# Kernel optimization log

Measured on AMD Instinct MI355X. Metric: run time of the kernel, lower is better.

Reference implementation:

```python
import jax, jax.numpy as jnp
import numpy as np

WINDOW_SIZE = 11
CHANNEL = 3
DATA_RANGE = 1.0
C1 = (0.01 * DATA_RANGE) ** 2
C2 = (0.03 * DATA_RANGE) ** 2


def _gaussian_window(window_size, channel, sigma=1.5):
    coords = np.arange(window_size, dtype=np.float32) - window_size // 2
    g = np.exp(-coords ** 2 / (2 * sigma ** 2))
    g = g / g.sum()
    g2d = g[:, None] * g[None, :]  # [K, K]
    # depthwise conv weight in OIHW with groups=channel -> [C, 1, K, K]
    w = np.broadcast_to(g2d[None, None], (channel, 1, window_size, window_size))
    return jnp.asarray(np.ascontiguousarray(w))


def _dwconv(x, w):
    # depthwise conv, stride 1, SAME padding (== pad window//2 for odd kernel)
    return jax.lax.conv_general_dilated(
        x, w, window_strides=(1, 1), padding='SAME',
        feature_group_count=x.shape[1],
        dimension_numbers=('NCHW', 'OIHW', 'NCHW'))


def setup_inputs() -> dict:
    key = jax.random.key(0)
    k1, k2 = jax.random.split(key)
    img1 = jax.random.normal(k1, (32, 3, 512, 512), dtype=jnp.float32)
    img2 = jax.random.normal(k2, (32, 3, 512, 512), dtype=jnp.float32)
    window = _gaussian_window(WINDOW_SIZE, CHANNEL)
    return {"img1": img1, "img2": img2, "window": window}


def reference(img1, img2, window):
    mu1 = _dwconv(img1, window)
    mu2 = _dwconv(img2, window)
    mu1_sq = mu1 * mu1
    mu2_sq = mu2 * mu2
    mu1_mu2 = mu1 * mu2
    sigma1_sq = jnp.maximum(_dwconv(img1 * img1, window) - mu1_sq, 0.0)
    sigma2_sq = jnp.maximum(_dwconv(img2 * img2, window) - mu2_sq, 0.0)
    sigma12 = _dwconv(img1 * img2, window) - mu1_mu2
    s1 = jnp.sqrt(sigma1_sq)
    s2 = jnp.sqrt(sigma2_sq)
    luminance = (2.0 * mu1_mu2 + C1) / (mu1_sq + mu2_sq + C1)
    contrast = (2.0 * s1 * s2 + C2) / (sigma1_sq + sigma2_sq + C2)
    structure = (sigma12 + C2 / 2) / (s1 * s2 + C2 / 2)
    ssim_map = luminance * contrast * structure
    return jnp.mean(ssim_map)
```

## Files before the change

### kernel.cpp

```cpp
#include <hip/hip_runtime.h>


#define IMG_H 512
#define IMG_W 512
#define N_IMGS 96
#define WAVE_W 64
#define STRIPE 128
#define HALO 5
#define KW 11
#define IN_COLS (WAVE_W + 2*HALO)
#define N_ROWT (IMG_H / STRIPE)
#define N_COLT (IMG_W / WAVE_W)
#define N_TILES (N_IMGS * N_ROWT * N_COLT)
#define WPB 4
#define N_BLOCKS (N_TILES / WPB)
#define T_MAX 143
#define NBINS 256
#define TOTAL_PIX (32.0f * 3.0f * 512.0f * 512.0f)

__global__ __launch_bounds__(64 * WPB)
void ssim_main(
    const float* __restrict__ img1, const float* __restrict__ img2,
    const float* __restrict__ window, float* __restrict__ bins)
{
    __shared__ float2 rowbuf_all[WPB][2][IN_COLS + 2];

    const int lane = threadIdx.x & 63;
    const int wv   = threadIdx.x >> 6;
    float2 (* __restrict__ rowbuf)[IN_COLS + 2] = rowbuf_all[wv];

    float g[KW];
    {
        const float inv = rsqrtf(window[5*KW + 5]);
        #pragma unroll
        for (int k = 0; k < KW; ++k)
            g[k] = __int_as_float(
                __builtin_amdgcn_readfirstlane(
                    __float_as_int(window[5*KW + k] * inv)));
    }

    const int b   = blockIdx.x * WPB + wv;
    const int img = b >> 5;
    const int rem = b & 31;
    const int ty  = rem >> 3;
    const int tx  = rem & 7;
    const int r0  = ty * STRIPE;
    const int x0  = tx * WAVE_W;

    const float* __restrict__ p1 = img1 + (size_t)img * (IMG_H * IMG_W);
    const float* __restrict__ p2 = img2 + (size_t)img * (IMG_H * IMG_W);

    const int  gx1  = x0 - HALO + lane;
    const bool c1ok = (unsigned)gx1 < IMG_W;
    const bool tail = lane < (IN_COLS - WAVE_W);
    const int  gx2  = gx1 + WAVE_W;
    const bool c2ok = tail && ((unsigned)gx2 < IMG_W);

    float r_h1[KW], r_h2[KW], r_h11[KW], r_h22[KW], r_h12[KW];
    #pragma unroll
    for (int i = 0; i < KW; ++i) {
        r_h1[i] = 0.f; r_h2[i] = 0.f; r_h11[i] = 0.f; r_h22[i] = 0.f; r_h12[i] = 0.f;
    }

    const float C1 = 1e-4f;
    const float C2 = 9e-4f;
    float sum = 0.f;

    float sa = 0.f, sb = 0.f, sa2 = 0.f, sb2 = 0.f;
    {
        const int gy = r0 - HALO;
        if ((unsigned)gy < IMG_H) {
            const int base = gy * IMG_W;
            if (c1ok) { sa  = p1[base + gx1]; sb  = p2[base + gx1]; }
            if (c2ok) { sa2 = p1[base + gx2]; sb2 = p2[base + gx2]; }
        }
    }

    #pragma unroll 1
    for (int tb = 0; tb < T_MAX; tb += KW) {
        #pragma unroll
        for (int u = 0; u < KW; ++u) {
            const int t = tb + u;

            rowbuf[u & 1][lane] = make_float2(sa, sb);
            if (tail) rowbuf[u & 1][lane + WAVE_W] = make_float2(sa2, sb2);

            asm volatile("" ::: "memory");

            {
                const int gy = r0 - HALO + t + 1;
                sa = 0.f; sb = 0.f; sa2 = 0.f; sb2 = 0.f;
                if ((unsigned)gy < IMG_H) {
                    const int base = gy * IMG_W;
                    if (c1ok) { sa  = p1[base + gx1]; sb  = p2[base + gx1]; }
                    if (c2ok) { sa2 = p1[base + gx2]; sb2 = p2[base + gx2]; }
                }
            }

            float h1 = 0.f, h2 = 0.f, h11 = 0.f, h22 = 0.f, h12 = 0.f;
            #pragma unroll
            for (int k = 0; k < KW; ++k) {
                const float2 v = rowbuf[u & 1][lane + k];
                const float t1 = g[k] * v.x;
                const float t2 = g[k] * v.y;
                h1  += t1;
                h2  += t2;
                h11 += t1 * v.x;
                h22 += t2 * v.y;
                h12 += t1 * v.y;
            }
            r_h1[u] = h1; r_h2[u] = h2; r_h11[u] = h11; r_h22[u] = h22; r_h12[u] = h12;

            if (t >= 2*HALO && t < 2*HALO + STRIPE) {
                float mu1 = 0.f, mu2 = 0.f, e11 = 0.f, e22 = 0.f, e12 = 0.f;
                #pragma unroll
                for (int m = 0; m < KW; ++m) {
                    const int slot = (u + 1 + m) % KW;
                    mu1 += g[m] * r_h1[slot];
                    mu2 += g[m] * r_h2[slot];
                    e11 += g[m] * r_h11[slot];
                    e22 += g[m] * r_h22[slot];
                    e12 += g[m] * r_h12[slot];
                }
                const float mu1s = mu1 * mu1, mu2s = mu2 * mu2, mu12 = mu1 * mu2;
                const float s1  = fmaxf(e11 - mu1s, 0.f);
                const float s2  = fmaxf(e22 - mu2s, 0.f);
                const float s12 = e12 - mu12;
                const float num = (2.f * mu12 + C1) * (2.f * s12 + C2);
                const float den = (mu1s + mu2s + C1) * (s1 + s2 + C2);
                sum += num * __builtin_amdgcn_rcpf(den);
            }
        }
    }

    #pragma unroll
    for (int off = 32; off > 0; off >>= 1)
        sum += __shfl_down(sum, off, 64);
    if (lane == 0)
        atomicAdd(&bins[b & (NBINS - 1)], sum);
}

__global__ __launch_bounds__(64) void ssim_final(
    const float* __restrict__ bins, float* __restrict__ out)
{
    const int tid = threadIdx.x;
    float s = 0.f;
    #pragma unroll
    for (int i = 0; i < NBINS / 64; ++i) s += bins[tid + i * 64];
    #pragma unroll
    for (int off = 32; off > 0; off >>= 1)
        s += __shfl_down(s, off, 64);
    if (tid == 0) out[0] = s * (1.0f / TOTAL_PIX);
}

extern "C" void kernel_launch(void* const* d_in, const int* in_sizes, int n_in,
                              void* d_out, int out_size, void* d_ws, size_t ws_size,
                              hipStream_t stream) {
    const float* img1   = (const float*)d_in[0];
    const float* img2   = (const float*)d_in[1];
    const float* window = (const float*)d_in[2];
    float* bins = (float*)d_ws;
    float* out  = (float*)d_out;

    hipMemsetAsync(bins, 0, NBINS * sizeof(float), stream);
    ssim_main<<<N_BLOCKS, 64 * WPB, 0, stream>>>(img1, img2, window, bins);
    ssim_final<<<1, 64, 0, stream>>>(bins, out);
}
```

Baseline: 318.7 us.

## Stream rows directly into LDS with async global_load_lds and 4-slot ring

Replaces register-staged row loads with direct global-to-LDS async loads (global_load_lds) into a 4-deep ring buffer, prefetching three rows ahead and waiting on vmcnt. Column indices are clamped and out-of-range halo columns are zeroed explicitly at image edges, while rows outside the image issue dummy loads to keep the vmcnt accounting constant. The row layout also changes from interleaved float2 to separate planes per image. The aim is deeper memory-latency hiding and less VGPR/LDS store traffic, at the cost of reliance on hand-coded waitcnt counts and races between zero-fill stores and in-flight async writes.

```diff
diff --git a/kernel.cpp b/kernel.cpp
--- a/kernel.cpp
+++ b/kernel.cpp
@@ -1,17 +1,16 @@
 #include <hip/hip_runtime.h>
+#include <stdint.h>
 
 
 #define IMG_H 512
 #define IMG_W 512
-#define N_IMGS 96
 #define WAVE_W 64
 #define STRIPE 128
 #define HALO 5
 #define KW 11
-#define IN_COLS (WAVE_W + 2*HALO)
 #define N_ROWT (IMG_H / STRIPE)
 #define N_COLT (IMG_W / WAVE_W)
-#define N_TILES (N_IMGS * N_ROWT * N_COLT)
+#define N_TILES (96 * N_ROWT * N_COLT)
 #define WPB 4
 #define N_BLOCKS (N_TILES / WPB)
 #define T_MAX 143
@@ -23,11 +22,13 @@
     const float* __restrict__ img1, const float* __restrict__ img2,
     const float* __restrict__ window, float* __restrict__ bins)
 {
-    __shared__ float2 rowbuf_all[WPB][2][IN_COLS + 2];
+    __shared__ float buf_all[WPB][4][2][128];
+    __shared__ float dump_all[WPB][64];
 
     const int lane = threadIdx.x & 63;
     const int wv   = threadIdx.x >> 6;
-    float2 (* __restrict__ rowbuf)[IN_COLS + 2] = rowbuf_all[wv];
+    float (* __restrict__ buf)[2][128] = buf_all[wv];
+    float* __restrict__ dump = dump_all[wv];
 
     float g[KW];
     {
@@ -50,11 +51,34 @@
     const float* __restrict__ p1 = img1 + (size_t)img * (IMG_H * IMG_W);
     const float* __restrict__ p2 = img2 + (size_t)img * (IMG_H * IMG_W);
 
-    const int  gx1  = x0 - HALO + lane;
-    const bool c1ok = (unsigned)gx1 < IMG_W;
-    const bool tail = lane < (IN_COLS - WAVE_W);
-    const int  gx2  = gx1 + WAVE_W;
-    const bool c2ok = tail && ((unsigned)gx2 < IMG_W);
+    const int cm = min(max(x0 - HALO + lane, 0), IMG_W - 1);
+    const int ct = min(max(x0 + WAVE_W - HALO + lane, 0), IMG_W - 1);
+
+    const float* pm1 = p1 + (long)(r0 - HALO) * IMG_W + cm;
+    const float* pm2 = p2 + (long)(r0 - HALO) * IMG_W + cm;
+    const float* pt1 = p1 + (long)(r0 - HALO) * IMG_W + ct;
+    const float* pt2 = p2 + (long)(r0 - HALO) * IMG_W + ct;
+    const float* pdm = p1 + lane;
+
+    auto issue = [&](int tl) {
+        const int slot = tl & 3;
+        float* s0 = &buf[slot][0][0];
+        float* s1 = &buf[slot][1][0];
+        if ((unsigned)(r0 - HALO + tl) < IMG_H) {
+            __builtin_amdgcn_global_load_lds(pm1, s0,      4, 0, 0);
+            __builtin_amdgcn_global_load_lds(pt1, s0 + 64, 4, 0, 0);
+            __builtin_amdgcn_global_load_lds(pm2, s1,      4, 0, 0);
+            __builtin_amdgcn_global_load_lds(pt2, s1 + 64, 4, 0, 0);
+        } else {
+            __builtin_amdgcn_global_load_lds(pdm, dump, 4, 0, 0);
+            __builtin_amdgcn_global_load_lds(pdm, dump, 4, 0, 0);
+            __builtin_amdgcn_global_load_lds(pdm, dump, 4, 0, 0);
+            __builtin_amdgcn_global_load_lds(pdm, dump, 4, 0, 0);
+            s0[lane] = 0.f; s0[64 + lane] = 0.f;
+            s1[lane] = 0.f; s1[64 + lane] = 0.f;
+        }
+        pm1 += IMG_W; pm2 += IMG_W; pt1 += IMG_W; pt2 += IMG_W;
+    };
 
     float r_h1[KW], r_h2[KW], r_h11[KW], r_h22[KW], r_h12[KW];
     #pragma unroll
@@ -66,15 +90,7 @@
     const float C2 = 9e-4f;
     float sum = 0.f;
 
-    float sa = 0.f, sb = 0.f, sa2 = 0.f, sb2 = 0.f;
-    {
-        const int gy = r0 - HALO;
-        if ((unsigned)gy < IMG_H) {
-            const int base = gy * IMG_W;
-            if (c1ok) { sa  = p1[base + gx1]; sb  = p2[base + gx1]; }
-            if (c2ok) { sa2 = p1[base + gx2]; sb2 = p2[base + gx2]; }
-        }
-    }
+    issue(0); issue(1); issue(2);
 
     #pragma unroll 1
     for (int tb = 0; tb < T_MAX; tb += KW) {
@@ -82,33 +98,40 @@
         for (int u = 0; u < KW; ++u) {
             const int t = tb + u;
 
-            rowbuf[u & 1][lane] = make_float2(sa, sb);
-            if (tail) rowbuf[u & 1][lane + WAVE_W] = make_float2(sa2, sb2);
+            issue(t + 3);
 
-            asm volatile("" ::: "memory");
+            asm volatile("s_waitcnt vmcnt(12)" ::: "memory");
 
-            {
-                const int gy = r0 - HALO + t + 1;
-                sa = 0.f; sb = 0.f; sa2 = 0.f; sb2 = 0.f;
-                if ((unsigned)gy < IMG_H) {
-                    const int base = gy * IMG_W;
-                    if (c1ok) { sa  = p1[base + gx1]; sb  = p2[base + gx1]; }
-                    if (c2ok) { sa2 = p1[base + gx2]; sb2 = p2[base + gx2]; }
+            if (tx == 0) {
+                if (lane < HALO) {
+                    buf[t & 3][0][lane] = 0.f;
+                    buf[t & 3][1][lane] = 0.f;
+                }
+            }
+            if (tx == 7) {
+                if (lane >= HALO && lane < 2*HALO) {
+                    buf[t & 3][0][64 + lane] = 0.f;
+                    buf[t & 3][1][64 + lane] = 0.f;
                 }
             }
 
+            const float* bA = &buf[t & 3][0][lane];
+            const float* bB = &buf[t & 3][1][lane];
             float h1 = 0.f, h2 = 0.f, h11 = 0.f, h22 = 0.f, h12 = 0.f;
             #pragma unroll
             for (int k = 0; k < KW; ++k) {
-                const float2 v = rowbuf[u & 1][lane + k];
-                const float t1 = g[k] * v.x;
-                const float t2 = g[k] * v.y;
+                const float va = bA[k];
+                const float vb = bB[k];
+                const float t1 = g[k] * va;
+                const float t2 = g[k] * vb;
                 h1  += t1;
                 h2  += t2;
-                h11 += t1 * v.x;
-                h22 += t2 * v.y;
-                h12 += t1 * v.y;
+                h11 += t1 * va;
+                h22 += t2 * vb;
+                h12 += t1 * vb;
             }
+            asm volatile("" ::: "memory");
+
             r_h1[u] = h1; r_h2[u] = h2; r_h11[u] = h11; r_h22[u] = h22; r_h12[u] = h12;
 
             if (t >= 2*HALO && t < 2*HALO + STRIPE) {
@@ -132,6 +155,8 @@
             }
         }
     }
+
+    asm volatile("s_waitcnt vmcnt(0)" ::: "memory");
 
     #pragma unroll
     for (int off = 32; off > 0; off >>= 1)
```

Result: slower. 329.9 us (+3.5%).
